# Kernel optimization log

Measured on AMD Instinct MI355X. Metric: run time of the kernel, lower is better.

Reference implementation:

```python
import jax, jax.numpy as jnp
import numpy as np

N, E, IN, H, B, OUT = 50000, 800000, 256, 64, 4096, 2
EPS, NEG = 0.3, 0.3  # eps residual coeff, LeakyReLU negative slope


def _xav(key, shape, gain=1.414):
    std = gain * np.sqrt(2.0 / (shape[0] + shape[1]))
    return jax.random.normal(key, shape, jnp.float32) * np.float32(std)


def setup_inputs():
    key = jax.random.key(0)
    ks = jax.random.split(key, 32)
    inp = {}
    inp["h"] = jax.random.normal(ks[0], (N, IN), jnp.float32)
    for i, name in enumerate(["src1", "dst1", "src2", "dst2", "src3", "dst3"]):
        inp[name] = jax.random.randint(ks[1 + i], (E,), 0, N, jnp.int32)
    inp["nodes"] = jax.random.randint(ks[7], (B,), 0, N, jnp.int32)
    inp["t1_w"] = _xav(ks[8], (H, IN))
    inp["t1_b"] = jnp.zeros((H,), jnp.float32)
    for i in range(3):
        inp[f"gw1_{i+1}"] = _xav(ks[9 + i], (1, 2 * H))
        inp[f"gb1_{i+1}"] = jnp.zeros((1,), jnp.float32)
        inp[f"hw1_{i+1}"] = _xav(ks[12 + i], (H, H))
        inp[f"gw2_{i+1}"] = _xav(ks[15 + i], (1, 6 * H))
        inp[f"gb2_{i+1}"] = jnp.zeros((1,), jnp.float32)
        inp[f"hw2_{i+1}"] = _xav(ks[18 + i], (3 * H, H))
    inp["t2_w"] = _xav(ks[21], (64, 7 * H + IN))
    inp["t2_b"] = jnp.zeros((64,), jnp.float32)
    inp["t3_w"] = _xav(ks[22], (OUT, 64))
    inp["t3_b"] = jnp.zeros((OUT,), jnp.float32)
    return inp


def _leaky(x):
    return jnp.where(x >= 0, x, NEG * x)


def _deg_norm(dst):
    # symmetric degree normalization d_i = 1/sqrt(deg_i) (FAGCN-style ndata['d'])
    deg = jax.ops.segment_sum(jnp.ones(dst.shape, jnp.float32), dst, num_segments=N)
    return jnp.where(deg > 0, jax.lax.rsqrt(jnp.maximum(deg, 1.0)), 0.0)


def _layer(h, src, dst, gw, gb, d):
    # a = tanh(gate(cat[h_dst, h_src])): split gate weight to avoid [E,2D] concat
    D = h.shape[1]
    a = jnp.tanh(h[dst] @ gw[0, :D] + h[src] @ gw[0, D:] + gb[0])  # [E]
    e = a * d[dst] * d[src]                                        # [E]
    # z_i = sum_{(src->i)} h_src * e  (DGL u_mul_e + sum)
    return jax.ops.segment_sum(h[src] * e[:, None], dst, num_segments=N)


def reference(h, t1_w, t1_b,
              gw1_1, gb1_1, hw1_1, gw1_2, gb1_2, hw1_2, gw1_3, gb1_3, hw1_3,
              gw2_1, gb2_1, hw2_1, gw2_2, gb2_2, hw2_2, gw2_3, gb2_3, hw2_3,
              t2_w, t2_b, t3_w, t3_b,
              src1, dst1, src2, dst2, src3, dst3, nodes):
    d1, d2, d3 = _deg_norm(dst1), _deg_norm(dst2), _deg_norm(dst3)
    raw0 = h
    x = _leaky(h @ t1_w.T + t1_b)                   # [N, H]
    raw1 = x
    h1_1 = _leaky((EPS * raw1 + _layer(x, src1, dst1, gw1_1, gb1_1, d1)) @ hw1_1)
    h1_2 = _leaky((EPS * raw1 + _layer(x, src2, dst2, gw1_2, gb1_2, d2)) @ hw1_2)
    h1_3 = _leaky((EPS * raw1 + _layer(x, src3, dst3, gw1_3, gb1_3, d3)) @ hw1_3)
    raw2 = jnp.concatenate([h1_1, h1_2, h1_3], axis=1)  # [N, 3H]
    h2_1 = _leaky((EPS * raw2 + _layer(raw2, src1, dst1, gw2_1, gb2_1, d1)) @ hw2_1)
    h2_2 = _leaky((EPS * raw2 + _layer(raw2, src2, dst2, gw2_2, gb2_2, d2)) @ hw2_2)
    h2_3 = _leaky((EPS * raw2 + _layer(raw2, src3, dst3, gw2_3, gb2_3, d3)) @ hw2_3)
    final = jnp.concatenate([h2_1, h2_2, h2_3, raw0, raw1, raw2], axis=1)  # [N, 7H+IN]
    nf = final[nodes]                                # [B, 7H+IN]
    s64 = _leaky(nf @ t2_w.T + t2_b)                 # [B, 64]
    scores = s64 @ t3_w.T + t3_b                     # [B, OUT]
    return scores, s64
```

## Files before the change

### kernel.cpp

```cpp
#include <hip/hip_runtime.h>

#define NN 50000
#define EE 800000
#define BB 4096
#define NB 512
#define BW 98
#define CAP 2176
#define CH 128

#define OFF_T1W 0
#define OFF_T1B 16384
#define OFF_GW1 16448
#define OFF_GB1 16832
#define OFF_HW1 16848
#define OFF_GW2 29136
#define OFF_GB2 30288
#define OFF_HW2 30304
#define OFF_T2W 67168
#define OFF_T2B 112224
#define OFF_T3W 112288
#define OFF_T3B 112416
#define WTOT    112418
#define WPAD    112640

#define WB_T1W  0
#define WB_HW1T 16384
#define WB_HW2T 28672
#define WB_T2W  65536
#define WB_TOT  110592

typedef __attribute__((ext_vector_type(8))) short bf16x8;
typedef __attribute__((ext_vector_type(4))) float f32x4;

__device__ __forceinline__ float bf2f(unsigned short u) {
    return __uint_as_float(((unsigned int)u) << 16);
}
__device__ __forceinline__ unsigned short f2bf(float f) {
    unsigned int u = __float_as_uint(f);
    u = (u + 0x7fffu + ((u >> 16) & 1u)) >> 16;
    return (unsigned short)u;
}
__device__ __forceinline__ float leakyf(float v) { return v >= 0.f ? v : 0.3f * v; }
__device__ __forceinline__ float tanh_fast(float v) {
    float e = __expf(2.f * v);
    return 1.f - 2.f / (e + 1.f);
}
__device__ __forceinline__ int rfl(int v) { return __builtin_amdgcn_readfirstlane(v); }

__device__ __forceinline__ int sniff_wave(const unsigned short* hs) {
    int lane = threadIdx.x & 63;
    unsigned short s = hs[2 * lane];
    int ef = (s >> 7) & 0xFF;
    unsigned long long m = __ballot(ef >= 100 && ef <= 132);
    return (__popcll(m) >= 40) ? 0 : 1;
}

__global__ __launch_bounds__(256) void k_convert(
    const unsigned short* __restrict__ hs,
    const void* t1w, const void* t1b,
    const void* gw1a, const void* gw1b, const void* gw1c,
    const void* gb1a, const void* gb1b, const void* gb1c,
    const void* hw1a, const void* hw1b, const void* hw1c,
    const void* gw2a, const void* gw2b, const void* gw2c,
    const void* gb2a, const void* gb2b, const void* gb2c,
    const void* hw2a, const void* hw2b, const void* hw2c,
    const void* t2w, const void* t2b, const void* t3w, const void* t3b,
    float* __restrict__ fw, unsigned short* __restrict__ wb) {
    const int starts[24] = {0, 16384, 16448, 16576, 16704, 16832, 16833, 16834,
                            16848, 20944, 25040, 29136, 29520, 29904, 30288, 30289, 30290,
                            30304, 42592, 54880, 67168, 112224, 112288, 112416};
    const int cnts[24] = {16384, 64, 128, 128, 128, 1, 1, 1, 4096, 4096, 4096,
                          384, 384, 384, 1, 1, 1, 12288, 12288, 12288, 45056, 64, 128, 2};
    const void* sp[24] = {t1w, t1b, gw1a, gw1b, gw1c, gb1a, gb1b, gb1c, hw1a, hw1b, hw1c,
                          gw2a, gw2b, gw2c, gb2a, gb2b, gb2c, hw2a, hw2b, hw2c, t2w, t2b, t3w, t3b};
    int isf32 = sniff_wave(hs);
    int idx = blockIdx.x * 256 + threadIdx.x;
    if (idx < WTOT) {
        float v = 0.f;
#pragma unroll
        for (int k = 0; k < 24; ++k) {
            int lo = idx - starts[k];
            if (lo >= 0 && lo < cnts[k])
                v = isf32 ? ((const float*)sp[k])[lo] : bf2f(((const unsigned short*)sp[k])[lo]);
        }
        fw[idx] = v;
    } else if (idx >= WPAD && idx < WPAD + WB_TOT) {
        int i2 = idx - WPAD;
        const void* p;
        int srci;
        if (i2 < WB_HW1T) {
            p = t1w; srci = i2;
        } else if (i2 < WB_HW2T) {
            int rel = i2 - WB_HW1T;
            int set = rel >> 12, r2 = rel & 4095;
            int jj = r2 >> 6, kk = r2 & 63;
            p = set == 0 ? hw1a : (set == 1 ? hw1b : hw1c);
            srci = kk * 64 + jj;
        } else if (i2 < WB_T2W) {
            int rel = i2 - WB_HW2T;
            int set = rel / 12288, r2 = rel % 12288;
            int n = r2 / 192, k = r2 % 192;
            p = set == 0 ? hw2a : (set == 1 ? hw2b : hw2c);
            srci = k * 64 + n;
        } else {
            p = t2w; srci = i2 - WB_T2W;
        }
        wb[i2] = isf32 ? f2bf(((const float*)p)[srci]) : ((const unsigned short*)p)[srci];
    }
}

__global__ __launch_bounds__(256) void k_bucketA(const int* __restrict__ s0, const int* __restrict__ s1,
                                                 const int* __restrict__ s2, const int* __restrict__ d0,
                                                 const int* __restrict__ d1, const int* __restrict__ d2,
                                                 int* __restrict__ gcur, unsigned int* __restrict__ tmp) {
    int set = blockIdx.y;
    const int* ss = set == 0 ? s0 : (set == 1 ? s1 : s2);
    const int* dd = set == 0 ? d0 : (set == 1 ? d1 : d2);
    __shared__ int hist[NB];
    __shared__ int lcur[NB];
    int tid = threadIdx.x;
    for (int i = tid; i < NB; i += 256) { hist[i] = 0; lcur[i] = 0; }
    __syncthreads();
    int e0 = blockIdx.x * (EE / CH);
    int e1 = e0 + (EE / CH);
    for (int t = e0 + tid; t < e1; t += 256)
        atomicAdd(&hist[dd[t] / BW], 1);
    __syncthreads();
    for (int b = tid; b < NB; b += 256) {
        int hh = hist[b];
        if (hh > 0) hist[b] = atomicAdd(&gcur[set * NB + b], hh);
    }
    __syncthreads();
    unsigned int* tp = tmp + (size_t)set * NB * CAP;
    for (int t = e0 + tid; t < e1; t += 256) {
        int d = dd[t], s = ss[t];
        int b = d / BW;
        int r = atomicAdd(&lcur[b], 1);
        int pos = hist[b] + r;
        if (pos < CAP) tp[(size_t)b * CAP + pos] = (unsigned)s | ((unsigned)(d - b * BW) << 16);
    }
}

__global__ __launch_bounds__(256) void k_rowptr(const int* __restrict__ gcur,
                                                const unsigned int* __restrict__ tmp,
                                                int* __restrict__ deg, int* __restrict__ rowptr,
                                                float* __restrict__ g1, float* __restrict__ g2) {
    int b = blockIdx.x, set = blockIdx.y;
    int nb = b * BW;
    if (nb >= NN) return;
    __shared__ int hist[BW];
    __shared__ int rp[BW];
    int tid = threadIdx.x;
    int nv = NN - nb < BW ? NN - nb : BW;
    if (tid < BW) hist[tid] = 0;
    __syncthreads();
    int cnt = gcur[set * NB + b];
    if (cnt > CAP) cnt = CAP;
    const unsigned int* tp = tmp + (size_t)set * NB * CAP + (size_t)b * CAP;
    for (int j = tid; j < cnt; j += 256) atomicAdd(&hist[tp[j] >> 16], 1);
    __syncthreads();
    if (tid == 0) {
        int run = 0;
        for (int i = 0; i < nv; ++i) { rp[i] = run; run += hist[i]; }
    }
    __syncthreads();
    if (tid < nv) {
        int dg = hist[tid];
        size_t n = (size_t)set * NN + nb + tid;
        deg[n] = dg;
        rowptr[n] = b * CAP + rp[tid];
        float v = dg > 0 ? rsqrtf((float)dg) : 0.f;
        g1[n * 4 + 2] = v;
        g2[n * 4 + 2] = v;
    }
}

__global__ __launch_bounds__(256) void k_input(const void* __restrict__ hB,
                                               const unsigned short* __restrict__ wb,
                                               const float* __restrict__ fw,
                                               unsigned short* __restrict__ x16,
                                               float4* __restrict__ g1v4) {
    __shared__ float xt[16][65];
    int tid = threadIdx.x, lane = tid & 63, wid = tid >> 6;
    int m = lane & 15, q = lane >> 4;
    int node0 = blockIdx.x * 16;
    int isf32 = sniff_wave((const unsigned short*)hB);
    f32x4 acc = {0.f, 0.f, 0.f, 0.f};
    const unsigned short* bsrc = wb + WB_T1W + ((size_t)(wid * 16 + m)) * 256 + q * 8;
    if (isf32) {
        const float* ap = (const float*)hB + (size_t)(node0 + m) * 256 + q * 8;
        for (int k0 = 0; k0 < 256; k0 += 32) {
            float4 f0 = *(const float4*)(ap + k0);
            float4 f1 = *(const float4*)(ap + k0 + 4);
            bf16x8 a;
            a[0] = (short)f2bf(f0.x); a[1] = (short)f2bf(f0.y);
            a[2] = (short)f2bf(f0.z); a[3] = (short)f2bf(f0.w);
            a[4] = (short)f2bf(f1.x); a[5] = (short)f2bf(f1.y);
            a[6] = (short)f2bf(f1.z); a[7] = (short)f2bf(f1.w);
            bf16x8 b = *(const bf16x8*)(bsrc + k0);
            acc = __builtin_amdgcn_mfma_f32_16x16x32_bf16(a, b, acc, 0, 0, 0);
        }
    } else {
        const unsigned short* ap = (const unsigned short*)hB + (size_t)(node0 + m) * 256 + q * 8;
        for (int k0 = 0; k0 < 256; k0 += 32) {
            bf16x8 a = *(const bf16x8*)(ap + k0);
            bf16x8 b = *(const bf16x8*)(bsrc + k0);
            acc = __builtin_amdgcn_mfma_f32_16x16x32_bf16(a, b, acc, 0, 0, 0);
        }
    }
    int gcol = wid * 16 + m;
    float bias = fw[OFF_T1B + gcol];
#pragma unroll
    for (int r = 0; r < 4; ++r) {
        int row = q * 4 + r;
        float v = leakyf(acc[r] + bias);
        x16[(size_t)(node0 + row) * 64 + gcol] = f2bf(v);
        xt[row][gcol] = v;
    }
    __syncthreads();
    int nl = wid * 4 + q;
    int node = node0 + nl;
    float xv[4];
#pragma unroll
    for (int r = 0; r < 4; ++r) xv[r] = xt[nl][m + 16 * r];
#pragma unroll
    for (int set = 0; set < 3; ++set) {
        const float* gw = fw + OFF_GW1 + set * 128;
        float pd = 0.f, ps = 0.f;
#pragma unroll
        for (int r = 0; r < 4; ++r) {
            int c = m + 16 * r;
            pd = fmaf(xv[r], gw[c], pd);
            ps = fmaf(xv[r], gw[64 + c], ps);
        }
        pd += __shfl_xor(pd, 1); ps += __shfl_xor(ps, 1);
        pd += __shfl_xor(pd, 2); ps += __shfl_xor(ps, 2);
        pd += __shfl_xor(pd, 4); ps += __shfl_xor(ps, 4);
        pd += __shfl_xor(pd, 8); ps += __shfl_xor(ps, 8);
        if (m == 0) {
            float2* p = (float2*)&g1v4[(size_t)set * NN + node];
            *p = make_float2(ps, pd);
        }
    }
}

__global__ __launch_bounds__(256) void k_bucketB(const int* __restrict__ gcur,
                                                 const unsigned int* __restrict__ tmp,
                                                 const int* __restrict__ rowptr,
                                                 const float4* __restrict__ g1v4,
                                                 const float* __restrict__ fw,
                                                 unsigned int* __restrict__ csr) {
    int b = blockIdx.x, set = blockIdx.y;
    int nb = b * BW;
    if (nb >= NN) return;
    __shared__ float4 gdw[BW];
    __shared__ int cur[BW];
    __shared__ int rpl[BW];
    int tid = threadIdx.x;
    int nv = NN - nb < BW ? NN - nb : BW;
    if (tid < nv) {
        gdw[tid] = g1v4[(size_t)set * NN + nb + tid];
        rpl[tid] = rowptr[(size_t)set * NN + nb + tid];
        cur[tid] = 0;
    }
    __syncthreads();
    int cnt = gcur[set * NB + b];
    if (cnt > CAP) cnt = CAP;
    float gbv = fw[OFF_GB1 + set];
    const float4* gv = g1v4 + (size_t)set * NN;
    const unsigned int* tp = tmp + (size_t)set * NB * CAP + (size_t)b * CAP;
    unsigned int* cp = csr + (size_t)set * NB * CAP;
    for (int j = tid; j < cnt; j += 256) {
        unsigned rec = tp[j];
        int s = rec & 0xFFFF;
        int dl = rec >> 16;
        float4 gs = gv[s];
        float4 gd = gdw[dl];
        float a = tanh_fast(gd.y + gs.x + gbv);
        float e = a * gd.z * gs.z;
        int rank = atomicAdd(&cur[dl], 1);
        cp[rpl[dl] + rank] = (unsigned)s | ((unsigned)f2bf(e) << 16);
    }
}

__global__ __launch_bounds__(1024) void k_layer1(const unsigned short* __restrict__ x16,
                                                 const unsigned int* __restrict__ csr,
                                                 const int* __restrict__ rowptr,
                                                 const int* __restrict__ deg,
                                                 const float* __restrict__ fw,
                                                 const unsigned short* __restrict__ wb,
                                                 unsigned short* __restrict__ raw2_16,
                                                 float4* __restrict__ g2v4) {
    __shared__ unsigned short tb[3][16][72];
    __shared__ unsigned short r2l[16][200];
    int tid = threadIdx.x, lane = tid & 63, wid = tid >> 6;
    int g = lane >> 4, f = lane & 15;
    int node = blockIdx.x * 16 + wid;
#pragma unroll
    for (int set = 0; set < 3; ++set) {
        int start = rfl(rowptr[(size_t)set * NN + node]);
        int cnt = rfl(deg[(size_t)set * NN + node]);
        const unsigned int* cs = csr + (size_t)set * NB * CAP + start;
        float a0 = 0.f, a1 = 0.f, a2 = 0.f, a3 = 0.f;
        int j = 0;
        for (; j + 8 <= cnt; j += 8) {
#pragma unroll
            for (int k2 = 0; k2 < 2; ++k2) {
                unsigned rec = cs[j + 4 * k2 + g];
                float e = bf2f((unsigned short)(rec >> 16));
                uint2 u = *(const uint2*)(x16 + (size_t)(rec & 0xFFFF) * 64 + 4 * f);
                a0 = fmaf(bf2f((unsigned short)(u.x & 0xFFFF)), e, a0);
                a1 = fmaf(bf2f((unsigned short)(u.x >> 16)), e, a1);
                a2 = fmaf(bf2f((unsigned short)(u.y & 0xFFFF)), e, a2);
                a3 = fmaf(bf2f((unsigned short)(u.y >> 16)), e, a3);
            }
        }
#pragma unroll
        for (int t = 0; t < 2; ++t) {
            int idx = j + 4 * t + g;
            if (idx < cnt) {
                unsigned rec = cs[idx];
                float e = bf2f((unsigned short)(rec >> 16));
                uint2 u = *(const uint2*)(x16 + (size_t)(rec & 0xFFFF) * 64 + 4 * f);
                a0 = fmaf(bf2f((unsigned short)(u.x & 0xFFFF)), e, a0);
                a1 = fmaf(bf2f((unsigned short)(u.x >> 16)), e, a1);
                a2 = fmaf(bf2f((unsigned short)(u.y & 0xFFFF)), e, a2);
                a3 = fmaf(bf2f((unsigned short)(u.y >> 16)), e, a3);
            }
        }
        a0 += __shfl_xor(a0, 16); a0 += __shfl_xor(a0, 32);
        a1 += __shfl_xor(a1, 16); a1 += __shfl_xor(a1, 32);
        a2 += __shfl_xor(a2, 16); a2 += __shfl_xor(a2, 32);
        a3 += __shfl_xor(a3, 16); a3 += __shfl_xor(a3, 32);
        if (g == 0) {
            uint2 ur = *(const uint2*)(x16 + (size_t)node * 64 + 4 * f);
            float t0 = fmaf(0.3f, bf2f((unsigned short)(ur.x & 0xFFFF)), a0);
            float t1 = fmaf(0.3f, bf2f((unsigned short)(ur.x >> 16)), a1);
            float t2 = fmaf(0.3f, bf2f((unsigned short)(ur.y & 0xFFFF)), a2);
            float t3 = fmaf(0.3f, bf2f((unsigned short)(ur.y >> 16)), a3);
            uint2 pk;
            pk.x = (unsigned)f2bf(t0) | ((unsigned)f2bf(t1) << 16);
            pk.y = (unsigned)f2bf(t2) | ((unsigned)f2bf(t3) << 16);
            *(uint2*)&tb[set][wid][4 * f] = pk;
        }
    }
    __syncthreads();
    int m = lane & 15, q = lane >> 4;
    if (wid < 12) {
        int set = wid >> 2, sw = wid & 3;
        f32x4 c4 = {0.f, 0.f, 0.f, 0.f};
        const unsigned short* bp = wb + WB_HW1T + set * 4096 + (sw * 16 + m) * 64 + q * 8;
#pragma unroll
        for (int k0 = 0; k0 < 64; k0 += 32) {
            bf16x8 a = *(const bf16x8*)&tb[set][m][k0 + q * 8];
            bf16x8 b = *(const bf16x8*)(bp + k0);
            c4 = __builtin_amdgcn_mfma_f32_16x16x32_bf16(a, b, c4, 0, 0, 0);
        }
        int gcol = sw * 16 + m;
#pragma unroll
        for (int r = 0; r < 4; ++r) {
            int row = q * 4 + r;
            unsigned short v = f2bf(leakyf(c4[r]));
            raw2_16[(size_t)(blockIdx.x * 16 + row) * 192 + set * 64 + gcol] = v;
            r2l[row][set * 64 + gcol] = v;
        }
    }
    __syncthreads();
    float pd[3] = {0.f, 0.f, 0.f}, ps[3] = {0.f, 0.f, 0.f};
    float rv[3];
#pragma unroll
    for (int t = 0; t < 3; ++t) rv[t] = bf2f(r2l[wid][lane * 3 + t]);
#pragma unroll
    for (int set = 0; set < 3; ++set) {
        const float* gg = fw + OFF_GW2 + set * 384;
#pragma unroll
        for (int t = 0; t < 3; ++t) {
            int cc = lane * 3 + t;
            pd[set] = fmaf(rv[t], gg[cc], pd[set]);
            ps[set] = fmaf(rv[t], gg[192 + cc], ps[set]);
        }
    }
#pragma unroll
    for (int mm = 32; mm >= 1; mm >>= 1) {
#pragma unroll
        for (int set = 0; set < 3; ++set) {
            pd[set] += __shfl_xor(pd[set], mm);
            ps[set] += __shfl_xor(ps[set], mm);
        }
    }
    if (lane == 0) {
#pragma unroll
        for (int set = 0; set < 3; ++set) {
            float2* p = (float2*)&g2v4[(size_t)set * NN + node];
            *p = make_float2(ps[set], pd[set]);
        }
    }
}

__global__ __launch_bounds__(1024) void k_final(const int* __restrict__ nodes,
                                                const unsigned short* __restrict__ raw2_16,
                                                const unsigned short* __restrict__ x16,
                                                const void* __restrict__ hB,
                                                const unsigned int* __restrict__ csr,
                                                const int* __restrict__ rowptr,
                                                const int* __restrict__ deg,
                                                const float4* __restrict__ g2v4,
                                                const float* __restrict__ fw,
                                                const unsigned short* __restrict__ wb,
                                                void* __restrict__ outv) {
    __shared__ unsigned short nfb[16][712];
    __shared__ unsigned short tbb3[16][584];
    __shared__ float sarr[16][64];
    __shared__ int nd[16];
    int tid = threadIdx.x, lane = tid & 63, wid = tid >> 6;
    int b0 = blockIdx.x * 16;
    int isf32 = sniff_wave((const unsigned short*)hB);
    if (tid < 16) nd[tid] = nodes[b0 + tid];
    __syncthreads();
    for (int idx = tid; idx < 16 * 256; idx += 1024) {
        int row = idx >> 8, c = idx & 255;
        size_t hi = (size_t)nd[row] * 256 + c;
        nfb[row][192 + c] = isf32 ? f2bf(((const float*)hB)[hi]) : ((const unsigned short*)hB)[hi];
    }
    for (int idx = tid; idx < 16 * 64; idx += 1024) {
        int row = idx >> 6, c = idx & 63;
        nfb[row][448 + c] = x16[(size_t)nd[row] * 64 + c];
    }
    for (int idx = tid; idx < 16 * 192; idx += 1024) {
        int row = idx / 192, c = idx % 192;
        nfb[row][512 + c] = raw2_16[(size_t)nd[row] * 192 + c];
    }
    __syncthreads();
    {
        int node = rfl(nd[wid]);
        int half = lane >> 5, c = lane & 31;
#pragma unroll
        for (int set = 0; set < 3; ++set) {
            int start = rfl(rowptr[(size_t)set * NN + node]);
            int cnt = rfl(deg[(size_t)set * NN + node]);
            float4 gn = g2v4[(size_t)set * NN + node];
            float pdv = gn.y, dnd = gn.z;
            float gbv = fw[OFF_GB2 + set];
            const unsigned int* cs = csr + (size_t)set * NB * CAP + start;
            const float4* gv = g2v4 + (size_t)set * NN;
            float a[6] = {0.f, 0.f, 0.f, 0.f, 0.f, 0.f};
            int j = 0;
            for (; j + 2 <= cnt; j += 2) {
                unsigned rec = cs[j + half];
                int s = rec & 0xFFFF;
                float4 gg = gv[s];
                float e = tanh_fast(pdv + gg.x + gbv) * dnd * gg.z;
                const unsigned short* r = raw2_16 + (size_t)s * 192;
#pragma unroll
                for (int blk = 0; blk < 3; ++blk) {
                    unsigned u = *(const unsigned*)(r + blk * 64 + 2 * c);
                    a[2 * blk] = fmaf(bf2f((unsigned short)(u & 0xFFFF)), e, a[2 * blk]);
                    a[2 * blk + 1] = fmaf(bf2f((unsigned short)(u >> 16)), e, a[2 * blk + 1]);
                }
            }
            if (j < cnt && half == 0) {
                unsigned rec = cs[j];
                int s = rec & 0xFFFF;
                float4 gg = gv[s];
                float e = tanh_fast(pdv + gg.x + gbv) * dnd * gg.z;
                const unsigned short* r = raw2_16 + (size_t)s * 192;
#pragma unroll
                for (int blk = 0; blk < 3; ++blk) {
                    unsigned u = *(const unsigned*)(r + blk * 64 + 2 * c);
                    a[2 * blk] = fmaf(bf2f((unsigned short)(u & 0xFFFF)), e, a[2 * blk]);
                    a[2 * blk + 1] = fmaf(bf2f((unsigned short)(u >> 16)), e, a[2 * blk + 1]);
                }
            }
#pragma unroll
            for (int i = 0; i < 6; ++i) a[i] += __shfl_xor(a[i], 32);
            if (half == 0) {
#pragma unroll
                for (int blk = 0; blk < 3; ++blk) {
                    int fc0 = blk * 64 + 2 * c;
                    float r20 = bf2f(nfb[wid][512 + fc0]);
                    float r21 = bf2f(nfb[wid][512 + fc0 + 1]);
                    tbb3[wid][set * 192 + fc0] = f2bf(fmaf(0.3f, r20, a[2 * blk]));
                    tbb3[wid][set * 192 + fc0 + 1] = f2bf(fmaf(0.3f, r21, a[2 * blk + 1]));
                }
            }
        }
    }
    __syncthreads();
    int m = lane & 15, q = lane >> 4;
    if (wid < 12) {
        int set = wid >> 2, sw = wid & 3;
        f32x4 c4 = {0.f, 0.f, 0.f, 0.f};
        const unsigned short* bp = wb + WB_HW2T + set * 12288 + (sw * 16 + m) * 192 + q * 8;
#pragma unroll
        for (int k0 = 0; k0 < 192; k0 += 32) {
            bf16x8 a = *(const bf16x8*)&tbb3[m][set * 192 + k0 + q * 8];
            bf16x8 bf = *(const bf16x8*)(bp + k0);
            c4 = __builtin_amdgcn_mfma_f32_16x16x32_bf16(a, bf, c4, 0, 0, 0);
        }
        int col = sw * 16 + m;
#pragma unroll
        for (int r = 0; r < 4; ++r)
            nfb[q * 4 + r][set * 64 + col] = f2bf(leakyf(c4[r]));
    }
    __syncthreads();
    if (wid < 4) {
        f32x4 c4 = {0.f, 0.f, 0.f, 0.f};
        const unsigned short* bp = wb + WB_T2W + (wid * 16 + m) * 704 + q * 8;
#pragma unroll
        for (int k0 = 0; k0 < 704; k0 += 32) {
            bf16x8 a = *(const bf16x8*)&nfb[m][k0 + q * 8];
            bf16x8 bf = *(const bf16x8*)(bp + k0);
            c4 = __builtin_amdgcn_mfma_f32_16x16x32_bf16(a, bf, c4, 0, 0, 0);
        }
        int col = wid * 16 + m;
        float bias = fw[OFF_T2B + col];
#pragma unroll
        for (int r = 0; r < 4; ++r) {
            int row = q * 4 + r;
            float sv = leakyf(c4[r] + bias);
            sarr[row][col] = sv;
            size_t oi = 8192 + (size_t)(b0 + row) * 64 + col;
            if (isf32) ((float*)outv)[oi] = sv;
            else ((unsigned short*)outv)[oi] = f2bf(sv);
        }
    }
    __syncthreads();
    if (tid < 32) {
        int row = tid >> 1, oc = tid & 1;
        float acc2 = fw[OFF_T3B + oc];
        const float* tw = fw + OFF_T3W + oc * 64;
#pragma unroll 8
        for (int c = 0; c < 64; ++c) acc2 = fmaf(sarr[row][c], tw[c], acc2);
        size_t oi = (size_t)(b0 + row) * 2 + oc;
        if (isf32) ((float*)outv)[oi] = acc2;
        else ((unsigned short*)outv)[oi] = f2bf(acc2);
    }
}

extern "C" void kernel_launch(void* const* d_in, const int* in_sizes, int n_in,
                              void* d_out, int out_size, void* d_ws, size_t ws_size,
                              hipStream_t stream) {
    const void* h = d_in[0];
    const int* src1 = (const int*)d_in[1];
    const int* dst1 = (const int*)d_in[2];
    const int* src2 = (const int*)d_in[3];
    const int* dst2 = (const int*)d_in[4];
    const int* src3 = (const int*)d_in[5];
    const int* dst3 = (const int*)d_in[6];
    const int* nodes = (const int*)d_in[7];

    char* w = (char*)d_ws;
    size_t off = 0;
    auto carve = [&](size_t bytes) -> void* {
        void* p = w + off;
        off += (bytes + 255) & ~(size_t)255;
        return p;
    };
    int* gcur = (int*)carve((size_t)3 * NB * 4);
    int* deg = (int*)carve((size_t)3 * NN * 4);
    int* rowptr = (int*)carve((size_t)3 * NN * 4);
    float4* g1v4 = (float4*)carve((size_t)3 * NN * 16);
    float4* g2v4 = (float4*)carve((size_t)3 * NN * 16);
    unsigned int* tmp = (unsigned int*)carve((size_t)3 * NB * CAP * 4);
    unsigned int* csr = (unsigned int*)carve((size_t)3 * NB * CAP * 4);
    float* fw = (float*)carve((size_t)WTOT * 4);
    unsigned short* wb = (unsigned short*)carve((size_t)WB_TOT * 2);
    unsigned short* x16 = (unsigned short*)carve((size_t)NN * 64 * 2);
    unsigned short* raw2_16 = (unsigned short*)carve((size_t)NN * 192 * 2);

    hipMemsetAsync(gcur, 0, (size_t)3 * NB * 4, stream);

    k_convert<<<(WPAD + WB_TOT) / 256, 256, 0, stream>>>(
        (const unsigned short*)h,
        d_in[8], d_in[9],
        d_in[10], d_in[16], d_in[22],
        d_in[11], d_in[17], d_in[23],
        d_in[12], d_in[18], d_in[24],
        d_in[13], d_in[19], d_in[25],
        d_in[14], d_in[20], d_in[26],
        d_in[15], d_in[21], d_in[27],
        d_in[28], d_in[29], d_in[30], d_in[31], fw, wb);

    dim3 gch(CH, 3);
    k_bucketA<<<gch, 256, 0, stream>>>(src1, src2, src3, dst1, dst2, dst3, gcur, tmp);
    dim3 gb(NB, 3);
    k_rowptr<<<gb, 256, 0, stream>>>(gcur, tmp, deg, rowptr, (float*)g1v4, (float*)g2v4);

    k_input<<<3125, 256, 0, stream>>>(h, wb, fw, x16, g1v4);
    k_bucketB<<<gb, 256, 0, stream>>>(gcur, tmp, rowptr, g1v4, fw, csr);

    k_layer1<<<3125, 1024, 0, stream>>>(x16, csr, rowptr, deg, fw, wb, raw2_16, g2v4);
    k_final<<<BB / 16, 1024, 0, stream>>>(nodes, raw2_16, x16, h, csr, rowptr, deg, g2v4,
                                          fw, wb, d_out);
}
```

Before: 377.8 us.

## Count degrees via global atomics in bucketing; simplify layer1 gather to per-lane features

Per-node degrees are now counted with global atomics during the first bucketing pass, so the rowptr kernel only reads them instead of rescanning the bucket temp buffer. The memset grows to cover the deg array. Separately, the layer-1 gather switches from a 4-edge-group, 4-feature-per-lane layout with shuffle reductions to one feature per lane over sequential edges, dropping the cross-group reductions but issuing narrower 2-byte loads and taking a longer serial dependency chain per wave. The global atomics add contention on 2.4M updates.

```diff
diff --git a/kernel.cpp b/kernel.cpp
--- a/kernel.cpp
+++ b/kernel.cpp
@@ -112,7 +112,8 @@
 __global__ __launch_bounds__(256) void k_bucketA(const int* __restrict__ s0, const int* __restrict__ s1,
                                                  const int* __restrict__ s2, const int* __restrict__ d0,
                                                  const int* __restrict__ d1, const int* __restrict__ d2,
-                                                 int* __restrict__ gcur, unsigned int* __restrict__ tmp) {
+                                                 int* __restrict__ gcur, int* __restrict__ deg,
+                                                 unsigned int* __restrict__ tmp) {
     int set = blockIdx.y;
     const int* ss = set == 0 ? s0 : (set == 1 ? s1 : s2);
     const int* dd = set == 0 ? d0 : (set == 1 ? d1 : d2);
@@ -123,8 +124,11 @@
     __syncthreads();
     int e0 = blockIdx.x * (EE / CH);
     int e1 = e0 + (EE / CH);
-    for (int t = e0 + tid; t < e1; t += 256)
-        atomicAdd(&hist[dd[t] / BW], 1);
+    for (int t = e0 + tid; t < e1; t += 256) {
+        int d = dd[t];
+        atomicAdd(&hist[d / BW], 1);
+        atomicAdd(&deg[(size_t)set * NN + d], 1);
+    }
     __syncthreads();
     for (int b = tid; b < NB; b += 256) {
         int hh = hist[b];
@@ -141,33 +145,25 @@
     }
 }
 
-__global__ __launch_bounds__(256) void k_rowptr(const int* __restrict__ gcur,
-                                                const unsigned int* __restrict__ tmp,
-                                                int* __restrict__ deg, int* __restrict__ rowptr,
+__global__ __launch_bounds__(128) void k_rowptr(const int* __restrict__ deg, int* __restrict__ rowptr,
                                                 float* __restrict__ g1, float* __restrict__ g2) {
     int b = blockIdx.x, set = blockIdx.y;
     int nb = b * BW;
     if (nb >= NN) return;
-    __shared__ int hist[BW];
+    __shared__ int dgs[BW];
     __shared__ int rp[BW];
     int tid = threadIdx.x;
     int nv = NN - nb < BW ? NN - nb : BW;
-    if (tid < BW) hist[tid] = 0;
-    __syncthreads();
-    int cnt = gcur[set * NB + b];
-    if (cnt > CAP) cnt = CAP;
-    const unsigned int* tp = tmp + (size_t)set * NB * CAP + (size_t)b * CAP;
-    for (int j = tid; j < cnt; j += 256) atomicAdd(&hist[tp[j] >> 16], 1);
+    if (tid < nv) dgs[tid] = deg[(size_t)set * NN + nb + tid];
     __syncthreads();
     if (tid == 0) {
         int run = 0;
-        for (int i = 0; i < nv; ++i) { rp[i] = run; run += hist[i]; }
+        for (int i = 0; i < nv; ++i) { rp[i] = run; run += dgs[i]; }
     }
     __syncthreads();
     if (tid < nv) {
-        int dg = hist[tid];
+        int dg = dgs[tid];
         size_t n = (size_t)set * NN + nb + tid;
-        deg[n] = dg;
         rowptr[n] = b * CAP + rp[tid];
         float v = dg > 0 ? rsqrtf((float)dg) : 0.f;
         g1[n * 4 + 2] = v;
@@ -294,55 +290,32 @@
     __shared__ unsigned short tb[3][16][72];
     __shared__ unsigned short r2l[16][200];
     int tid = threadIdx.x, lane = tid & 63, wid = tid >> 6;
-    int g = lane >> 4, f = lane & 15;
     int node = blockIdx.x * 16 + wid;
+    float xr = bf2f(x16[(size_t)node * 64 + lane]);
 #pragma unroll
     for (int set = 0; set < 3; ++set) {
         int start = rfl(rowptr[(size_t)set * NN + node]);
         int cnt = rfl(deg[(size_t)set * NN + node]);
         const unsigned int* cs = csr + (size_t)set * NB * CAP + start;
-        float a0 = 0.f, a1 = 0.f, a2 = 0.f, a3 = 0.f;
+        float acc = 0.f;
         int j = 0;
-        for (; j + 8 <= cnt; j += 8) {
-#pragma unroll
-            for (int k2 = 0; k2 < 2; ++k2) {
-                unsigned rec = cs[j + 4 * k2 + g];
-                float e = bf2f((unsigned short)(rec >> 16));
-                uint2 u = *(const uint2*)(x16 + (size_t)(rec & 0xFFFF) * 64 + 4 * f);
-                a0 = fmaf(bf2f((unsigned short)(u.x & 0xFFFF)), e, a0);
-                a1 = fmaf(bf2f((unsigned short)(u.x >> 16)), e, a1);
-                a2 = fmaf(bf2f((unsigned short)(u.y & 0xFFFF)), e, a2);
-                a3 = fmaf(bf2f((unsigned short)(u.y >> 16)), e, a3);
-            }
-        }
-#pragma unroll
-        for (int t = 0; t < 2; ++t) {
-            int idx = j + 4 * t + g;
-            if (idx < cnt) {
-                unsigned rec = cs[idx];
-                float e = bf2f((unsigned short)(rec >> 16));
-                uint2 u = *(const uint2*)(x16 + (size_t)(rec & 0xFFFF) * 64 + 4 * f);
-                a0 = fmaf(bf2f((unsigned short)(u.x & 0xFFFF)), e, a0);
-                a1 = fmaf(bf2f((unsigned short)(u.x >> 16)), e, a1);
-                a2 = fmaf(bf2f((unsigned short)(u.y & 0xFFFF)), e, a2);
-                a3 = fmaf(bf2f((unsigned short)(u.y >> 16)), e, a3);
-            }
-        }
-        a0 += __shfl_xor(a0, 16); a0 += __shfl_xor(a0, 32);
-        a1 += __shfl_xor(a1, 16); a1 += __shfl_xor(a1, 32);
-        a2 += __shfl_xor(a2, 16); a2 += __shfl_xor(a2, 32);
-        a3 += __shfl_xor(a3, 16); a3 += __shfl_xor(a3, 32);
-        if (g == 0) {
-            uint2 ur = *(const uint2*)(x16 + (size_t)node * 64 + 4 * f);
-            float t0 = fmaf(0.3f, bf2f((unsigned short)(ur.x & 0xFFFF)), a0);
-            float t1 = fmaf(0.3f, bf2f((unsigned short)(ur.x >> 16)), a1);
-            float t2 = fmaf(0.3f, bf2f((unsigned short)(ur.y & 0xFFFF)), a2);
-            float t3 = fmaf(0.3f, bf2f((unsigned short)(ur.y >> 16)), a3);
-            uint2 pk;
-            pk.x = (unsigned)f2bf(t0) | ((unsigned)f2bf(t1) << 16);
-            pk.y = (unsigned)f2bf(t2) | ((unsigned)f2bf(t3) << 16);
-            *(uint2*)&tb[set][wid][4 * f] = pk;
-        }
+        for (; j + 4 <= cnt; j += 4) {
+            unsigned r0 = cs[j], r1 = cs[j + 1], r2 = cs[j + 2], r3 = cs[j + 3];
+            float v0 = bf2f(x16[(size_t)(r0 & 0xFFFF) * 64 + lane]);
+            float v1 = bf2f(x16[(size_t)(r1 & 0xFFFF) * 64 + lane]);
+            float v2 = bf2f(x16[(size_t)(r2 & 0xFFFF) * 64 + lane]);
+            float v3 = bf2f(x16[(size_t)(r3 & 0xFFFF) * 64 + lane]);
+            acc = fmaf(v0, bf2f((unsigned short)(r0 >> 16)), acc);
+            acc = fmaf(v1, bf2f((unsigned short)(r1 >> 16)), acc);
+            acc = fmaf(v2, bf2f((unsigned short)(r2 >> 16)), acc);
+            acc = fmaf(v3, bf2f((unsigned short)(r3 >> 16)), acc);
+        }
+        for (; j < cnt; ++j) {
+            unsigned r0 = cs[j];
+            acc = fmaf(bf2f(x16[(size_t)(r0 & 0xFFFF) * 64 + lane]),
+                       bf2f((unsigned short)(r0 >> 16)), acc);
+        }
+        tb[set][wid][lane] = f2bf(fmaf(0.3f, xr, acc));
     }
     __syncthreads();
     int m = lane & 15, q = lane >> 4;
@@ -568,7 +541,8 @@
     unsigned short* x16 = (unsigned short*)carve((size_t)NN * 64 * 2);
     unsigned short* raw2_16 = (unsigned short*)carve((size_t)NN * 192 * 2);
 
-    hipMemsetAsync(gcur, 0, (size_t)3 * NB * 4, stream);
+    size_t zbytes = (size_t)((char*)rowptr - (char*)gcur);
+    hipMemsetAsync(gcur, 0, zbytes, stream);
 
     k_convert<<<(WPAD + WB_TOT) / 256, 256, 0, stream>>>(
         (const unsigned short*)h,
@@ -582,9 +556,9 @@
         d_in[28], d_in[29], d_in[30], d_in[31], fw, wb);
 
     dim3 gch(CH, 3);
-    k_bucketA<<<gch, 256, 0, stream>>>(src1, src2, src3, dst1, dst2, dst3, gcur, tmp);
+    k_bucketA<<<gch, 256, 0, stream>>>(src1, src2, src3, dst1, dst2, dst3, gcur, deg, tmp);
     dim3 gb(NB, 3);
-    k_rowptr<<<gb, 256, 0, stream>>>(gcur, tmp, deg, rowptr, (float*)g1v4, (float*)g2v4);
+    k_rowptr<<<gb, 128, 0, stream>>>(deg, rowptr, (float*)g1v4, (float*)g2v4);
 
     k_input<<<3125, 256, 0, stream>>>(h, wb, fw, x16, g1v4);
     k_bucketB<<<gb, 256, 0, stream>>>(gcur, tmp, rowptr, g1v4, fw, csr);
```

Result: slower. 454.4 us (+20.3%).
